# Kernel tuning notes

Hardware: AMD Instinct MI355X
Metric: run time of the kernel (lower is better)

Reference implementation:

```python
import jax, jax.numpy as jnp
import numpy as np

D_MODEL = 2048
NUM_HEADS = 16
D_K = D_MODEL // NUM_HEADS
B, S, PAST = 2, 1024, 3072


def setup_inputs() -> dict:
    key = jax.random.key(0)
    ks = jax.random.split(key, 12)
    s = 1.0 / np.sqrt(D_MODEL)
    inp = {
        "x": jax.random.normal(ks[0], (B, S, D_MODEL), dtype=jnp.float32),
        "past_key": jax.random.normal(ks[1], (B, NUM_HEADS, PAST, D_K), dtype=jnp.float32),
        "past_value": jax.random.normal(ks[2], (B, NUM_HEADS, PAST, D_K), dtype=jnp.float32),
        "Wq": jax.random.normal(ks[3], (D_MODEL, D_MODEL), dtype=jnp.float32) * s,
        "bq": jax.random.normal(ks[4], (D_MODEL,), dtype=jnp.float32) * s,
        "Wk": jax.random.normal(ks[5], (D_MODEL, D_MODEL), dtype=jnp.float32) * s,
        "bk": jax.random.normal(ks[6], (D_MODEL,), dtype=jnp.float32) * s,
        "Wv": jax.random.normal(ks[7], (D_MODEL, D_MODEL), dtype=jnp.float32) * s,
        "bv": jax.random.normal(ks[8], (D_MODEL,), dtype=jnp.float32) * s,
        "Wo": jax.random.normal(ks[9], (D_MODEL, D_MODEL), dtype=jnp.float32) * s,
        "bo": jax.random.normal(ks[10], (D_MODEL,), dtype=jnp.float32) * s,
    }
    return inp


def reference(x, past_key, past_value, Wq, bq, Wk, bk, Wv, bv, Wo, bo):
    b, s, _ = x.shape
    # torch nn.Linear: y = x @ W^T + b
    def proj(W, bias):
        y = jnp.einsum('bsd,ed->bse', x, W) + bias
        return y.reshape(b, s, NUM_HEADS, D_K).transpose(0, 2, 1, 3)  # [B,H,S,dk]
    Q = proj(Wq, bq)
    K = proj(Wk, bk)
    V = proj(Wv, bv)
    K = jnp.concatenate([past_key, K], axis=2)   # [B,H,PAST+S,dk]
    V = jnp.concatenate([past_value, V], axis=2)
    scale = 1.0 / np.sqrt(D_K).astype(np.float32)
    scores = jnp.einsum('bhqd,bhkd->bhqk', Q, K) * scale
    attn = jax.nn.softmax(scores, axis=-1)
    out = jnp.einsum('bhqk,bhkd->bhqd', attn, V)          # [B,H,S,dk]
    out = out.transpose(0, 2, 1, 3).reshape(b, s, D_MODEL)
    out = jnp.einsum('bsd,ed->bse', out, Wo) + bo
    return out, K, V
```

## Files before the change

kernel.cpp:

```cpp
#include <hip/hip_runtime.h>
#include <stdint.h>

typedef __bf16 bf16;
typedef __bf16 bf16x4 __attribute__((ext_vector_type(4)));
typedef __bf16 bf16x8 __attribute__((ext_vector_type(8)));
typedef float  f32x4  __attribute__((ext_vector_type(4)));

#define DMODEL 2048
#define NH 16
#define DK 128
#define SS 1024
#define PASTLEN 3072
#define LTOT 4096
#define KVTILES 64
#define NSPLIT 2
#define NT 32

__device__ __forceinline__ void gload16(const void* g, void* l) {
    __builtin_amdgcn_global_load_lds(
        (__attribute__((address_space(1))) void*)(uintptr_t)g,
        (__attribute__((address_space(3))) void*)(uintptr_t)l,
        16, 0, 0);
}

__global__ __launch_bounds__(256) void cvt5_k(
    const float* __restrict__ s0, const float* __restrict__ s1,
    const float* __restrict__ s2, const float* __restrict__ s3,
    const float* __restrict__ s4,
    bf16* __restrict__ d0, bf16* __restrict__ d1, bf16* __restrict__ d2,
    bf16* __restrict__ d3, bf16* __restrict__ d4, int n8)
{
    const float* s; bf16* d;
    switch (blockIdx.y) {
        case 0: s = s0; d = d0; break;
        case 1: s = s1; d = d1; break;
        case 2: s = s2; d = d2; break;
        case 3: s = s3; d = d3; break;
        default: s = s4; d = d4; break;
    }
    int stride = gridDim.x * blockDim.x;
    for (int i = blockIdx.x*blockDim.x + threadIdx.x; i < n8; i += stride) {
        const float4* p = (const float4*)s + (size_t)i*2;
        float4 a = p[0], b = p[1];
        bf16x8 o;
        o[0]=(bf16)a.x; o[1]=(bf16)a.y; o[2]=(bf16)a.z; o[3]=(bf16)a.w;
        o[4]=(bf16)b.x; o[5]=(bf16)b.y; o[6]=(bf16)b.z; o[7]=(bf16)b.w;
        *((bf16x8*)d + i) = o;
    }
}

__global__ __launch_bounds__(256) void gemm_bt(
    const bf16* __restrict__ A,
    const bf16* __restrict__ W0, const bf16* __restrict__ W1, const bf16* __restrict__ W2,
    const float* __restrict__ b0, const float* __restrict__ b1, const float* __restrict__ b2,
    bf16* __restrict__ outQ, float* __restrict__ outK, float* __restrict__ outV,
    float* __restrict__ outO, int mode)
{
    __shared__ __align__(16) bf16 As[128*32];
    __shared__ __align__(16) bf16 Bs[128*32];
    const int tid  = threadIdx.x;
    const int wave = tid >> 6, lane = tid & 63;
    const int l15 = lane & 15, l4 = lane >> 4;
    int which, ntile;
    if (mode == 0) { which = blockIdx.y >> 4; ntile = blockIdx.y & 15; }
    else           { which = 3;               ntile = blockIdx.y; }
    const bf16*  W    = (mode != 0 || which == 0) ? W0 : (which == 1 ? W1 : W2);
    const float* bias = (mode != 0 || which == 0) ? b0 : (which == 1 ? b1 : b2);
    const int m0 = blockIdx.x * 128, n0 = ntile * 128;
    const int wm = wave >> 1, wn = wave & 1;

    f32x4 acc[4][4] = {};

    for (int k0 = 0; k0 < DMODEL; k0 += 32) {
        __syncthreads();
        #pragma unroll
        for (int c = 0; c < 2; ++c) {
            const int base = c*4096 + wave*1024;
            const int byte = base + lane*16;
            const int row  = byte >> 6;
            const int ke   = (byte & 63) >> 1;
            gload16(A + (size_t)(m0+row)*DMODEL + k0 + ke, (char*)As + base);
            gload16(W + (size_t)(n0+row)*DMODEL + k0 + ke, (char*)Bs + base);
        }
        asm volatile("s_waitcnt vmcnt(0)" ::: "memory");
        __syncthreads();
        bf16x8 af[4], bfv[4];
        #pragma unroll
        for (int mf = 0; mf < 4; ++mf)
            af[mf] = *(const bf16x8*)((const char*)As + (wm*64 + mf*16 + l15)*64 + l4*16);
        #pragma unroll
        for (int nf = 0; nf < 4; ++nf)
            bfv[nf] = *(const bf16x8*)((const char*)Bs + (wn*64 + nf*16 + l15)*64 + l4*16);
        #pragma unroll
        for (int mf = 0; mf < 4; ++mf)
            #pragma unroll
            for (int nf = 0; nf < 4; ++nf)
                acc[mf][nf] = __builtin_amdgcn_mfma_f32_16x16x32_bf16(af[mf], bfv[nf], acc[mf][nf], 0, 0, 0);
    }

    float bv4[4];
    #pragma unroll
    for (int nf = 0; nf < 4; ++nf) bv4[nf] = bias[n0 + wn*64 + nf*16 + l15];

    const int rbase = m0 + wm*64 + l4*4;
    const int cbase = n0 + wn*64 + l15;

    if (mode == 1) {
        #pragma unroll
        for (int mf = 0; mf < 4; ++mf)
        #pragma unroll
        for (int nf = 0; nf < 4; ++nf) {
            const int col = cbase + nf*16;
            #pragma unroll
            for (int r = 0; r < 4; ++r) {
                const int row = rbase + mf*16 + r;
                outO[(size_t)row*DMODEL + col] = acc[mf][nf][r] + bv4[nf];
            }
        }
    } else if (which == 0) {
        const float qs = 0.08838834764831845f * 1.4426950408889634f;
        #pragma unroll
        for (int mf = 0; mf < 4; ++mf)
        #pragma unroll
        for (int nf = 0; nf < 4; ++nf) {
            const int col = cbase + nf*16;
            const int h = col >> 7, d = col & 127;
            #pragma unroll
            for (int r = 0; r < 4; ++r) {
                const int row = rbase + mf*16 + r;
                const int b = row >> 10, s = row & 1023;
                outQ[((size_t)(b*NH + h)*SS + s)*DK + d] = (bf16)((acc[mf][nf][r] + bv4[nf]) * qs);
            }
        }
    } else {
        float* dst = (which == 1) ? outK : outV;
        #pragma unroll
        for (int mf = 0; mf < 4; ++mf)
        #pragma unroll
        for (int nf = 0; nf < 4; ++nf) {
            const int col = cbase + nf*16;
            const int h = col >> 7, d = col & 127;
            #pragma unroll
            for (int r = 0; r < 4; ++r) {
                const int row = rbase + mf*16 + r;
                const int b = row >> 10, s = row & 1023;
                dst[((size_t)(b*NH + h)*LTOT + PASTLEN + s)*DK + d] = acc[mf][nf][r] + bv4[nf];
            }
        }
    }
}

__global__ __launch_bounds__(256) void kvprep_k(
    const float* __restrict__ pk, const float* __restrict__ pv,
    float* __restrict__ Kf, float* __restrict__ Vf,
    bf16* __restrict__ Kb, bf16* __restrict__ Vb)
{
    __shared__ float Vt_f[64*132];
    const int tid = threadIdx.x;
    const int tau = blockIdx.x, bh = blockIdx.y;
    const bool past = tau < 48;
    const size_t srcoff = past ? ((size_t)bh*PASTLEN + tau*64)*DK
                               : ((size_t)bh*LTOT    + tau*64)*DK;
    const float* srcK = (past ? pk : Kf) + srcoff;
    const float* srcV = (past ? pv : Vf) + srcoff;
    float* dstKf = Kf + ((size_t)bh*LTOT + tau*64)*DK;
    float* dstVf = Vf + ((size_t)bh*LTOT + tau*64)*DK;
    char* kblob = (char*)Kb + (((size_t)bh*KVTILES + tau) << 14);
    char* vblob = (char*)Vb + (((size_t)bh*KVTILES + tau) << 14);

    #pragma unroll
    for (int i = 0; i < 8; ++i) {
        const int f4 = i*256 + tid;
        const int r  = f4 >> 5;
        const int c8 = f4 & 31;
        float4 k4 = ((const float4*)srcK)[f4];
        float4 v4 = ((const float4*)srcV)[f4];
        if (past) {
            ((float4*)dstKf)[f4] = k4;
            ((float4*)dstVf)[f4] = v4;
        }
        bf16x4 kq; kq[0]=(bf16)k4.x; kq[1]=(bf16)k4.y; kq[2]=(bf16)k4.z; kq[3]=(bf16)k4.w;
        *(bf16x4*)(kblob + r*256 + ((c8*8) ^ ((r&7)<<4))) = kq;
        *(float4*)&Vt_f[r*132 + c8*4] = v4;
    }
    __syncthreads();
    const int d = tid >> 1, half = tid & 1;
    const int dx = (d & 7) << 4;
    #pragma unroll
    for (int j = 0; j < 4; ++j) {
        const int chunk = half*4 + j;
        bf16x8 o;
        #pragma unroll
        for (int e = 0; e < 8; ++e) o[e] = (bf16)Vt_f[(chunk*8 + e)*132 + d];
        *(bf16x8*)(vblob + d*128 + ((chunk*16) ^ dx)) = o;
    }
}

__global__ __launch_bounds__(512, 2) void attn_k(
    const bf16* __restrict__ Qb,
    const bf16* __restrict__ Kb, const bf16* __restrict__ Vb,
    bf16* __restrict__ Opart, float* __restrict__ Marr, float* __restrict__ Larr)
{
    __shared__ __align__(16) char KL[2][16384];
    __shared__ __align__(16) char VL[2][16384];
    __shared__ __align__(16) char PsL[8][4096];

    const int tid  = threadIdx.x;
    const int wave = tid >> 6, lane = tid & 63;
    const int l15 = lane & 15, l4 = lane >> 4;
    const int qt = blockIdx.x & 3;
    const int sp = blockIdx.x >> 2;
    const int bh = blockIdx.y;
    const int qbase = qt*256 + wave*32;

    bf16x8 qf[2][4];
    #pragma unroll
    for (int qq = 0; qq < 2; ++qq) {
        const bf16* qptr = Qb + ((size_t)bh*SS + qbase + qq*16 + l15)*DK;
        #pragma unroll
        for (int ks = 0; ks < 4; ++ks)
            qf[qq][ks] = *(const bf16x8*)(qptr + ks*32 + l4*8);
    }

    const char* kblobs = (const char*)Kb + (((size_t)bh*KVTILES + sp*NT) << 14);
    const char* vblobs = (const char*)Vb + (((size_t)bh*KVTILES + sp*NT) << 14);
    char* myPs = PsL[wave];
    const int soff = wave*2048;

    float m_run[2][4], l_run[2][4];
    f32x4 oacc[2][8];
    #pragma unroll
    for (int qq = 0; qq < 2; ++qq) {
        #pragma unroll
        for (int r = 0; r < 4; ++r) { m_run[qq][r] = -1e30f; l_run[qq][r] = 0.f; }
        #pragma unroll
        for (int df = 0; df < 8; ++df) oacc[qq][df] = f32x4{0.f,0.f,0.f,0.f};
    }

    #pragma unroll
    for (int c = 0; c < 2; ++c) {
        const int off = soff + c*1024;
        gload16(kblobs + off + lane*16, KL[0] + off);
        gload16(vblobs + off + lane*16, VL[0] + off);
    }

    for (int t = 0; t < NT; ++t) {
        const int cur = t & 1;
        if (t + 1 < NT) {
            const char* kb = kblobs + ((size_t)(t+1) << 14);
            const char* vb = vblobs + ((size_t)(t+1) << 14);
            #pragma unroll
            for (int c = 0; c < 2; ++c) {
                const int off = soff + c*1024;
                gload16(kb + off + lane*16, KL[cur^1] + off);
                gload16(vb + off + lane*16, VL[cur^1] + off);
            }
            asm volatile("s_waitcnt vmcnt(4)" ::: "memory");
        } else {
            asm volatile("s_waitcnt vmcnt(0)" ::: "memory");
        }
        __builtin_amdgcn_s_barrier();
        asm volatile("" ::: "memory");

        const char* Kc = KL[cur];
        const char* Vc = VL[cur];

        f32x4 sa[2][4];
        #pragma unroll
        for (int qq = 0; qq < 2; ++qq)
            #pragma unroll
            for (int nf = 0; nf < 4; ++nf) sa[qq][nf] = f32x4{0.f,0.f,0.f,0.f};
        __builtin_amdgcn_s_setprio(1);
        #pragma unroll
        for (int nf = 0; nf < 4; ++nf) {
            const int krow = nf*16 + l15;
            const int rx = (krow & 7) << 4;
            #pragma unroll
            for (int ks = 0; ks < 4; ++ks) {
                bf16x8 kf = *(const bf16x8*)(Kc + krow*256 + ((ks*64 + l4*16) ^ rx));
                sa[0][nf] = __builtin_amdgcn_mfma_f32_16x16x32_bf16(qf[0][ks], kf, sa[0][nf], 0,0,0);
                sa[1][nf] = __builtin_amdgcn_mfma_f32_16x16x32_bf16(qf[1][ks], kf, sa[1][nf], 0,0,0);
            }
        }
        __builtin_amdgcn_s_setprio(0);

        #pragma unroll
        for (int qq = 0; qq < 2; ++qq) {
            #pragma unroll
            for (int r = 0; r < 4; ++r) {
                float mt = fmaxf(fmaxf(sa[qq][0][r], sa[qq][1][r]),
                                 fmaxf(sa[qq][2][r], sa[qq][3][r]));
                #pragma unroll
                for (int off = 1; off < 16; off <<= 1) mt = fmaxf(mt, __shfl_xor(mt, off, 64));
                const float mn   = fmaxf(m_run[qq][r], mt);
                const float corr = exp2f(m_run[qq][r] - mn);
                m_run[qq][r] = mn;
                float sum = 0.f;
                #pragma unroll
                for (int nf = 0; nf < 4; ++nf) {
                    float p = exp2f(sa[qq][nf][r] - mn);
                    sa[qq][nf][r] = p;
                    sum += p;
                }
                #pragma unroll
                for (int off = 1; off < 16; off <<= 1) sum += __shfl_xor(sum, off, 64);
                l_run[qq][r] = l_run[qq][r]*corr + sum;
                #pragma unroll
                for (int df = 0; df < 8; ++df) oacc[qq][df][r] *= corr;
            }
            #pragma unroll
            for (int nf = 0; nf < 4; ++nf)
                #pragma unroll
                for (int r = 0; r < 4; ++r) {
                    const int row = qq*16 + l4*4 + r;
                    *(bf16*)(myPs + row*128 + (((nf*16 + l15)*2) ^ ((row&7)<<4))) = (bf16)sa[qq][nf][r];
                }
        }

        bf16x8 pf[2][2];
        #pragma unroll
        for (int qq = 0; qq < 2; ++qq) {
            const int prow = qq*16 + l15;
            const int px = (prow & 7) << 4;
            #pragma unroll
            for (int ks2 = 0; ks2 < 2; ++ks2)
                pf[qq][ks2] = *(const bf16x8*)(myPs + prow*128 + ((ks2*64 + l4*16) ^ px));
        }
        __builtin_amdgcn_s_setprio(1);
        #pragma unroll
        for (int ks2 = 0; ks2 < 2; ++ks2) {
            #pragma unroll
            for (int df = 0; df < 8; ++df) {
                const int d = df*16 + l15;
                bf16x8 vf = *(const bf16x8*)(Vc + d*128 + ((ks2*64 + l4*16) ^ ((d&7)<<4)));
                oacc[0][df] = __builtin_amdgcn_mfma_f32_16x16x32_bf16(pf[0][ks2], vf, oacc[0][df], 0,0,0);
                oacc[1][df] = __builtin_amdgcn_mfma_f32_16x16x32_bf16(pf[1][ks2], vf, oacc[1][df], 0,0,0);
            }
        }
        __builtin_amdgcn_s_setprio(0);

        asm volatile("" ::: "memory");
        __builtin_amdgcn_s_barrier();
    }

    bf16* op = Opart + ((size_t)sp*32 + bh)*SS*DK;
    #pragma unroll
    for (int qq = 0; qq < 2; ++qq)
        #pragma unroll
        for (int df = 0; df < 8; ++df)
            #pragma unroll
            for (int r = 0; r < 4; ++r) {
                const int q = qbase + qq*16 + l4*4 + r;
                op[(size_t)q*DK + df*16 + l15] = (bf16)oacc[qq][df][r];
            }
    if (l15 == 0) {
        #pragma unroll
        for (int qq = 0; qq < 2; ++qq)
            #pragma unroll
            for (int r = 0; r < 4; ++r) {
                const int q = qbase + qq*16 + l4*4 + r;
                Marr[(size_t)sp*32768 + bh*SS + q] = m_run[qq][r];
                Larr[(size_t)sp*32768 + bh*SS + q] = l_run[qq][r];
            }
    }
}

__global__ __launch_bounds__(256) void combine_k(
    const bf16* __restrict__ Opart, const float* __restrict__ Marr,
    const float* __restrict__ Larr, bf16* __restrict__ Ob)
{
    const int gid = blockIdx.x*256 + threadIdx.x;
    const int row = gid >> 4;
    const int c8  = gid & 15;
    const int bh = row >> 10, q = row & 1023;
    const float m0 = Marr[row], m1 = Marr[32768 + row];
    const float l0 = Larr[row], l1 = Larr[32768 + row];
    const float M = fmaxf(m0, m1);
    float a0 = exp2f(m0 - M), a1 = exp2f(m1 - M);
    const float inv = 1.f / (l0*a0 + l1*a1);
    a0 *= inv; a1 *= inv;
    bf16x8 p0 = *(const bf16x8*)(Opart + (size_t)row*DK + c8*8);
    bf16x8 p1 = *(const bf16x8*)(Opart + 4194304 + (size_t)row*DK + c8*8);
    const int b = bh >> 4, h = bh & 15;
    bf16x8 o;
    #pragma unroll
    for (int e = 0; e < 8; ++e) o[e] = (bf16)((float)p0[e]*a0 + (float)p1[e]*a1);
    *(bf16x8*)(Ob + ((size_t)(b*SS + q))*DMODEL + h*DK + c8*8) = o;
}

extern "C" void kernel_launch(void* const* d_in, const int* in_sizes, int n_in,
                              void* d_out, int out_size, void* d_ws, size_t ws_size,
                              hipStream_t stream) {
    const float* x  = (const float*)d_in[0];
    const float* pk = (const float*)d_in[1];
    const float* pv = (const float*)d_in[2];
    const float* Wq = (const float*)d_in[3];
    const float* bq = (const float*)d_in[4];
    const float* Wk = (const float*)d_in[5];
    const float* bk = (const float*)d_in[6];
    const float* Wv = (const float*)d_in[7];
    const float* bv = (const float*)d_in[8];
    const float* Wo = (const float*)d_in[9];
    const float* bo = (const float*)d_in[10];

    float* out  = (float*)d_out;
    float* Kout = out + 4194304;
    float* Vout = out + 20971520;

    char* ws = (char*)d_ws;
    bf16* xb    = (bf16*)(ws);
    bf16* Wqb   = (bf16*)(ws + (size_t)8*1024*1024);
    bf16* Wkb   = (bf16*)(ws + (size_t)16*1024*1024);
    bf16* Wvb   = (bf16*)(ws + (size_t)24*1024*1024);
    bf16* Wob   = (bf16*)(ws + (size_t)32*1024*1024);
    bf16* Qb    = (bf16*)(ws + (size_t)40*1024*1024);
    bf16* Ob    = (bf16*)(ws + (size_t)48*1024*1024);
    bf16* Kb    = (bf16*)(ws + (size_t)56*1024*1024);
    bf16* Vb    = (bf16*)(ws + (size_t)88*1024*1024);
    bf16*  Opart = (bf16*)(ws);
    float* Marr  = (float*)(ws + (size_t)24*1024*1024);
    float* Larr  = (float*)(ws + (size_t)25*1024*1024);

    cvt5_k<<<dim3(1024, 5), 256, 0, stream>>>(x, Wq, Wk, Wv, Wo,
                                              xb, Wqb, Wkb, Wvb, Wob, 524288);
    gemm_bt<<<dim3(16, 48), 256, 0, stream>>>(xb, Wqb, Wkb, Wvb, bq, bk, bv,
                                              Qb, Kout, Vout, nullptr, 0);
    kvprep_k<<<dim3(64, 32), 256, 0, stream>>>(pk, pv, Kout, Vout, Kb, Vb);
    attn_k<<<dim3(8, 32), 512, 0, stream>>>(Qb, Kb, Vb, Opart, Marr, Larr);
    combine_k<<<2048, 256, 0, stream>>>(Opart, Marr, Larr, Ob);
    gemm_bt<<<dim3(16, 16), 256, 0, stream>>>(Ob, Wob, nullptr, nullptr, bo, nullptr, nullptr,
                                              nullptr, nullptr, nullptr, out, 1);
}
```

Measured before the change: 337.1 us.

## Split attention KV four ways, single-buffer V, lazy rescale, MFMA row sums

Doubles the KV split of the attention kernel to four, giving twice as many workgroups, and raises the occupancy hint. V is now single-buffered with its load issued at the start of each tile and waited on just before the PV MFMAs, which frees LDS for more resident blocks. The online softmax rescales only when some row max grows by more than a threshold, and the row sum is computed with an MFMA against a ones vector instead of shuffle reductions. The combine kernel generalises to NSPLIT partials, and the M/L scratch arrays move into the output buffer ahead of the final GEMM, which overwrites them. In exchange the combine step reads twice as much partial data, and the deferred rescale lets probabilities exceed one before conversion to bf16.

After: 767.9 us. 2.28x slower.

```diff
diff --git a/kernel.cpp b/kernel.cpp
--- a/kernel.cpp
+++ b/kernel.cpp
@@ -13,8 +13,8 @@
 #define PASTLEN 3072
 #define LTOT 4096
 #define KVTILES 64
-#define NSPLIT 2
-#define NT 32
+#define NSPLIT 4
+#define NT 16
 
 __device__ __forceinline__ void gload16(const void* g, void* l) {
     __builtin_amdgcn_global_load_lds(
@@ -196,13 +196,13 @@
     }
 }
 
-__global__ __launch_bounds__(512, 2) void attn_k(
+__global__ __launch_bounds__(512, 4) void attn_k(
     const bf16* __restrict__ Qb,
     const bf16* __restrict__ Kb, const bf16* __restrict__ Vb,
     bf16* __restrict__ Opart, float* __restrict__ Marr, float* __restrict__ Larr)
 {
     __shared__ __align__(16) char KL[2][16384];
-    __shared__ __align__(16) char VL[2][16384];
+    __shared__ __align__(16) char VL[16384];
     __shared__ __align__(16) char PsL[8][4096];
 
     const int tid  = threadIdx.x;
@@ -227,43 +227,43 @@
     char* myPs = PsL[wave];
     const int soff = wave*2048;
 
-    float m_run[2][4], l_run[2][4];
+    bf16x8 ones8;
+    #pragma unroll
+    for (int e = 0; e < 8; ++e) ones8[e] = (bf16)1.0f;
+
+    float m_run[2][4];
     f32x4 oacc[2][8];
+    f32x4 lacc[2];
     #pragma unroll
     for (int qq = 0; qq < 2; ++qq) {
         #pragma unroll
-        for (int r = 0; r < 4; ++r) { m_run[qq][r] = -1e30f; l_run[qq][r] = 0.f; }
+        for (int r = 0; r < 4; ++r) m_run[qq][r] = -1e30f;
         #pragma unroll
         for (int df = 0; df < 8; ++df) oacc[qq][df] = f32x4{0.f,0.f,0.f,0.f};
-    }
-
-    #pragma unroll
-    for (int c = 0; c < 2; ++c) {
-        const int off = soff + c*1024;
-        gload16(kblobs + off + lane*16, KL[0] + off);
-        gload16(vblobs + off + lane*16, VL[0] + off);
-    }
+        lacc[qq] = f32x4{0.f,0.f,0.f,0.f};
+    }
+
+    #pragma unroll
+    for (int c = 0; c < 2; ++c)
+        gload16(kblobs + soff + c*1024 + lane*16, KL[0] + soff + c*1024);
 
     for (int t = 0; t < NT; ++t) {
         const int cur = t & 1;
+        #pragma unroll
+        for (int c = 0; c < 2; ++c)
+            gload16(vblobs + ((size_t)t << 14) + soff + c*1024 + lane*16, VL + soff + c*1024);
         if (t + 1 < NT) {
             const char* kb = kblobs + ((size_t)(t+1) << 14);
-            const char* vb = vblobs + ((size_t)(t+1) << 14);
-            #pragma unroll
-            for (int c = 0; c < 2; ++c) {
-                const int off = soff + c*1024;
-                gload16(kb + off + lane*16, KL[cur^1] + off);
-                gload16(vb + off + lane*16, VL[cur^1] + off);
-            }
+            #pragma unroll
+            for (int c = 0; c < 2; ++c)
+                gload16(kb + soff + c*1024 + lane*16, KL[cur^1] + soff + c*1024);
             asm volatile("s_waitcnt vmcnt(4)" ::: "memory");
         } else {
-            asm volatile("s_waitcnt vmcnt(0)" ::: "memory");
+            asm volatile("s_waitcnt vmcnt(2)" ::: "memory");
         }
         __builtin_amdgcn_s_barrier();
-        asm volatile("" ::: "memory");
 
         const char* Kc = KL[cur];
-        const char* Vc = VL[cur];
 
         f32x4 sa[2][4];
         #pragma unroll
@@ -284,38 +284,42 @@
         }
         __builtin_amdgcn_s_setprio(0);
 
-        #pragma unroll
-        for (int qq = 0; qq < 2; ++qq) {
-            #pragma unroll
-            for (int r = 0; r < 4; ++r) {
-                float mt = fmaxf(fmaxf(sa[qq][0][r], sa[qq][1][r]),
+        float mt[2][4];
+        bool ok = true;
+        #pragma unroll
+        for (int qq = 0; qq < 2; ++qq)
+            #pragma unroll
+            for (int r = 0; r < 4; ++r) {
+                float m0 = fmaxf(fmaxf(sa[qq][0][r], sa[qq][1][r]),
                                  fmaxf(sa[qq][2][r], sa[qq][3][r]));
                 #pragma unroll
-                for (int off = 1; off < 16; off <<= 1) mt = fmaxf(mt, __shfl_xor(mt, off, 64));
-                const float mn   = fmaxf(m_run[qq][r], mt);
-                const float corr = exp2f(m_run[qq][r] - mn);
-                m_run[qq][r] = mn;
-                float sum = 0.f;
+                for (int off = 1; off < 16; off <<= 1) m0 = fmaxf(m0, __shfl_xor(m0, off, 64));
+                mt[qq][r] = m0;
+                ok = ok && (m0 <= m_run[qq][r] + 8.0f);
+            }
+        if (!__all(ok)) {
+            #pragma unroll
+            for (int qq = 0; qq < 2; ++qq)
                 #pragma unroll
-                for (int nf = 0; nf < 4; ++nf) {
-                    float p = exp2f(sa[qq][nf][r] - mn);
-                    sa[qq][nf][r] = p;
-                    sum += p;
+                for (int r = 0; r < 4; ++r) {
+                    const float mn   = fmaxf(m_run[qq][r], mt[qq][r]);
+                    const float corr = exp2f(m_run[qq][r] - mn);
+                    m_run[qq][r] = mn;
+                    #pragma unroll
+                    for (int df = 0; df < 8; ++df) oacc[qq][df][r] *= corr;
+                    lacc[qq][r] *= corr;
                 }
-                #pragma unroll
-                for (int off = 1; off < 16; off <<= 1) sum += __shfl_xor(sum, off, 64);
-                l_run[qq][r] = l_run[qq][r]*corr + sum;
-                #pragma unroll
-                for (int df = 0; df < 8; ++df) oacc[qq][df][r] *= corr;
-            }
+        }
+        #pragma unroll
+        for (int qq = 0; qq < 2; ++qq)
             #pragma unroll
             for (int nf = 0; nf < 4; ++nf)
                 #pragma unroll
                 for (int r = 0; r < 4; ++r) {
+                    const float p = exp2f(sa[qq][nf][r] - m_run[qq][r]);
                     const int row = qq*16 + l4*4 + r;
-                    *(bf16*)(myPs + row*128 + (((nf*16 + l15)*2) ^ ((row&7)<<4))) = (bf16)sa[qq][nf][r];
+                    *(bf16*)(myPs + row*128 + (((nf*16 + l15)*2) ^ ((row&7)<<4))) = (bf16)p;
                 }
-        }
 
         bf16x8 pf[2][2];
         #pragma unroll
@@ -326,20 +330,26 @@
             for (int ks2 = 0; ks2 < 2; ++ks2)
                 pf[qq][ks2] = *(const bf16x8*)(myPs + prow*128 + ((ks2*64 + l4*16) ^ px));
         }
+
+        if (t + 1 < NT) asm volatile("s_waitcnt vmcnt(2)" ::: "memory");
+        else            asm volatile("s_waitcnt vmcnt(0)" ::: "memory");
+        __builtin_amdgcn_s_barrier();
+
         __builtin_amdgcn_s_setprio(1);
         #pragma unroll
         for (int ks2 = 0; ks2 < 2; ++ks2) {
+            lacc[0] = __builtin_amdgcn_mfma_f32_16x16x32_bf16(pf[0][ks2], ones8, lacc[0], 0,0,0);
+            lacc[1] = __builtin_amdgcn_mfma_f32_16x16x32_bf16(pf[1][ks2], ones8, lacc[1], 0,0,0);
             #pragma unroll
             for (int df = 0; df < 8; ++df) {
                 const int d = df*16 + l15;
-                bf16x8 vf = *(const bf16x8*)(Vc + d*128 + ((ks2*64 + l4*16) ^ ((d&7)<<4)));
+                bf16x8 vf = *(const bf16x8*)(VL + d*128 + ((ks2*64 + l4*16) ^ ((d&7)<<4)));
                 oacc[0][df] = __builtin_amdgcn_mfma_f32_16x16x32_bf16(pf[0][ks2], vf, oacc[0][df], 0,0,0);
                 oacc[1][df] = __builtin_amdgcn_mfma_f32_16x16x32_bf16(pf[1][ks2], vf, oacc[1][df], 0,0,0);
             }
         }
         __builtin_amdgcn_s_setprio(0);
 
-        asm volatile("" ::: "memory");
         __builtin_amdgcn_s_barrier();
     }
 
@@ -360,7 +370,7 @@
             for (int r = 0; r < 4; ++r) {
                 const int q = qbase + qq*16 + l4*4 + r;
                 Marr[(size_t)sp*32768 + bh*SS + q] = m_run[qq][r];
-                Larr[(size_t)sp*32768 + bh*SS + q] = l_run[qq][r];
+                Larr[(size_t)sp*32768 + bh*SS + q] = lacc[qq][r];
             }
     }
 }
@@ -373,18 +383,32 @@
     const int row = gid >> 4;
     const int c8  = gid & 15;
     const int bh = row >> 10, q = row & 1023;
-    const float m0 = Marr[row], m1 = Marr[32768 + row];
-    const float l0 = Larr[row], l1 = Larr[32768 + row];
-    const float M = fmaxf(m0, m1);
-    float a0 = exp2f(m0 - M), a1 = exp2f(m1 - M);
-    const float inv = 1.f / (l0*a0 + l1*a1);
-    a0 *= inv; a1 *= inv;
-    bf16x8 p0 = *(const bf16x8*)(Opart + (size_t)row*DK + c8*8);
-    bf16x8 p1 = *(const bf16x8*)(Opart + 4194304 + (size_t)row*DK + c8*8);
+    float m[NSPLIT], l[NSPLIT];
+    #pragma unroll
+    for (int s = 0; s < NSPLIT; ++s) {
+        m[s] = Marr[(size_t)s*32768 + row];
+        l[s] = Larr[(size_t)s*32768 + row];
+    }
+    float M = m[0];
+    #pragma unroll
+    for (int s = 1; s < NSPLIT; ++s) M = fmaxf(M, m[s]);
+    float w[NSPLIT], den = 0.f;
+    #pragma unroll
+    for (int s = 0; s < NSPLIT; ++s) { w[s] = exp2f(m[s] - M); den += l[s]*w[s]; }
+    const float inv = 1.f / den;
+    #pragma unroll
+    for (int s = 0; s < NSPLIT; ++s) w[s] *= inv;
+    float acc[8] = {};
+    #pragma unroll
+    for (int s = 0; s < NSPLIT; ++s) {
+        bf16x8 p = *(const bf16x8*)(Opart + (size_t)s*4194304 + (size_t)row*DK + c8*8);
+        #pragma unroll
+        for (int e = 0; e < 8; ++e) acc[e] += (float)p[e]*w[s];
+    }
     const int b = bh >> 4, h = bh & 15;
     bf16x8 o;
     #pragma unroll
-    for (int e = 0; e < 8; ++e) o[e] = (bf16)((float)p0[e]*a0 + (float)p1[e]*a1);
+    for (int e = 0; e < 8; ++e) o[e] = (bf16)acc[e];
     *(bf16x8*)(Ob + ((size_t)(b*SS + q))*DMODEL + h*DK + c8*8) = o;
 }
 
@@ -418,15 +442,15 @@
     bf16* Kb    = (bf16*)(ws + (size_t)56*1024*1024);
     bf16* Vb    = (bf16*)(ws + (size_t)88*1024*1024);
     bf16*  Opart = (bf16*)(ws);
-    float* Marr  = (float*)(ws + (size_t)24*1024*1024);
-    float* Larr  = (float*)(ws + (size_t)25*1024*1024);
+    float* Marr  = out;
+    float* Larr  = out + 131072;
 
     cvt5_k<<<dim3(1024, 5), 256, 0, stream>>>(x, Wq, Wk, Wv, Wo,
                                               xb, Wqb, Wkb, Wvb, Wob, 524288);
     gemm_bt<<<dim3(16, 48), 256, 0, stream>>>(xb, Wqb, Wkb, Wvb, bq, bk, bv,
                                               Qb, Kout, Vout, nullptr, 0);
     kvprep_k<<<dim3(64, 32), 256, 0, stream>>>(pk, pv, Kout, Vout, Kb, Vb);
-    attn_k<<<dim3(8, 32), 512, 0, stream>>>(Qb, Kb, Vb, Opart, Marr, Larr);
+    attn_k<<<dim3(16, 32), 512, 0, stream>>>(Qb, Kb, Vb, Opart, Marr, Larr);
     combine_k<<<2048, 256, 0, stream>>>(Opart, Marr, Larr, Ob);
     gemm_bt<<<dim3(16, 16), 256, 0, stream>>>(Ob, Wob, nullptr, nullptr, bo, nullptr, nullptr,
                                               nullptr, nullptr, nullptr, out, 1);
```
